# Performance work log

Hardware: AMD Instinct MI355X
Metric: run time of the kernel (lower is better)

## Reference

```python
import jax, jax.numpy as jnp
import numpy as np
from jax import lax

B, H, W, C = 8, 256, 256, 64
REDUCTION = 8
LENGTH = 9
HIDDEN = max(8, C // REDUCTION)


def _conv(x, w, b, pad='SAME'):
    y = lax.conv_general_dilated(x, w, (1, 1), pad,
                                 dimension_numbers=('NHWC', 'HWIO', 'NHWC'))
    return y + b


def _bilinear_sample(img, y, x):
    # img: [B,H,W,C]; y,x: [B,H,W] float coords
    Bi, Hi, Wi, _ = img.shape
    y0 = jnp.floor(y)
    x0 = jnp.floor(x)
    y0i = jnp.clip(y0.astype(jnp.int32), 0, Hi - 1)
    x0i = jnp.clip(x0.astype(jnp.int32), 0, Wi - 1)
    y1i = jnp.clip((y0 + 1.0).astype(jnp.int32), 0, Hi - 1)
    x1i = jnp.clip((x0 + 1.0).astype(jnp.int32), 0, Wi - 1)
    b = jnp.arange(Bi)[:, None, None]
    Ia = img[b, y0i, x0i]
    Ib = img[b, y1i, x0i]
    Ic = img[b, y0i, x1i]
    Id = img[b, y1i, x1i]
    # weights use CLIPPED integer corner coords (faithful to the TF source)
    y0f = y0i.astype(img.dtype)
    x0f = x0i.astype(img.dtype)
    y1f = y1i.astype(img.dtype)
    x1f = x1i.astype(img.dtype)
    wa = ((x1f - x) * (y1f - y))[..., None]
    wb = ((x1f - x) * (y - y0f))[..., None]
    wc = ((x - x0f) * (y1f - y))[..., None]
    wd = ((x - x0f) * (y - y0f))[..., None]
    return wa * Ia + wb * Ib + wc * Ic + wd * Id


def _oriented_pool(x, vx, vy):
    # x: [B,H,W,C]; vx,vy: [B,H,W] unit direction components
    _, Hi, Wi, _ = x.shape
    yy = jnp.arange(Hi, dtype=x.dtype)[None, :, None]  # broadcasts to [B,H,W]
    xx = jnp.arange(Wi, dtype=x.dtype)[None, None, :]
    half = LENGTH // 2
    acc = jnp.zeros_like(x)
    for t in range(-half, half + 1):  # fixed small set of offsets
        tf_ = jnp.asarray(t, dtype=x.dtype)
        cy = yy + tf_ * vy
        cx = xx + tf_ * vx
        acc = acc + _bilinear_sample(x, cy, cx)
    return acc / jnp.asarray(LENGTH, dtype=x.dtype)


def setup_inputs() -> dict:
    key = jax.random.key(0)
    ks = jax.random.split(key, 9)
    s = 0.05
    return {
        'x': jax.random.normal(ks[0], (B, H, W, C), jnp.float32),
        'w3': jax.random.normal(ks[1], (3, 3, C, HIDDEN), jnp.float32) * s,
        'b3': jnp.zeros((HIDDEN,), jnp.float32),
        'w1': jax.random.normal(ks[2], (1, 1, HIDDEN, 1), jnp.float32) * s,
        'b1': jnp.zeros((1,), jnp.float32),
        'wr': jax.random.normal(ks[3], (1, 1, 2 * C, HIDDEN), jnp.float32) * s,
        'br': jnp.zeros((HIDDEN,), jnp.float32),
        'we': jax.random.normal(ks[4], (1, 1, HIDDEN, 2 * C), jnp.float32) * s,
        'be': jnp.zeros((2 * C,), jnp.float32),
    }


def reference(x, w3, b3, w1, b1, wr, br, we, be):
    h = jax.nn.relu(_conv(x, w3, b3))                    # [B,H,W,hidden]
    theta = np.pi * jax.nn.sigmoid(_conv(h, w1, b1))     # [B,H,W,1]
    cos_t = jnp.cos(theta)[..., 0]                       # [B,H,W]
    sin_t = jnp.sin(theta)[..., 0]
    tan_feat = _oriented_pool(x, cos_t, sin_t)           # tangential direction
    nor_feat = _oriented_pool(x, -sin_t, cos_t)          # normal direction
    context = jnp.concatenate([tan_feat, nor_feat], axis=-1)  # [B,H,W,2C]
    r = jax.nn.relu(_conv(context, wr, br))
    w = jax.nn.sigmoid(_conv(r, we, be))                 # [B,H,W,2C]
    alpha_tan, alpha_norm = jnp.split(w, 2, axis=-1)
    return (alpha_tan + alpha_norm) * x
```

## Files before the change

### kernel.cpp

```cpp
#include <hip/hip_runtime.h>
#include <math.h>

#define PI_F 3.14159265358979323846f

typedef float f2 __attribute__((ext_vector_type(2)));

__device__ __forceinline__ f2 pkfma(f2 a, f2 b, f2 c) {
    return __builtin_elementwise_fma(a, b, c);
}
__device__ __forceinline__ f2 sp(float v) { f2 r; r.x = v; r.y = v; return r; }
__device__ __forceinline__ f2 mk2(float a, float b) { f2 r; r.x = a; r.y = b; return r; }

__device__ __forceinline__ float fold8h(float v0, float v1, float v2, float v3,
                                        float v4, float v5, float v6, float v7,
                                        int hl) {
    const bool b4 = (hl & 4) != 0;
    float k0 = b4 ? v4 : v0, g0 = b4 ? v0 : v4;
    float k1 = b4 ? v5 : v1, g1 = b4 ? v1 : v5;
    float k2 = b4 ? v6 : v2, g2 = b4 ? v2 : v6;
    float k3 = b4 ? v7 : v3, g3 = b4 ? v3 : v7;
    k0 += __shfl_xor(g0, 4, 64);
    k1 += __shfl_xor(g1, 4, 64);
    k2 += __shfl_xor(g2, 4, 64);
    k3 += __shfl_xor(g3, 4, 64);
    const bool b2 = (hl & 2) != 0;
    float m0 = b2 ? k2 : k0, n0 = b2 ? k0 : k2;
    float m1 = b2 ? k3 : k1, n1 = b2 ? k1 : k3;
    m0 += __shfl_xor(n0, 2, 64);
    m1 += __shfl_xor(n1, 2, 64);
    const bool b1_ = (hl & 1) != 0;
    float q = b1_ ? m1 : m0, r = b1_ ? m0 : m1;
    q += __shfl_xor(r, 1, 64);
    q += __shfl_xor(q, 8, 64);
    q += __shfl_xor(q, 16, 64);
    return q;
}

__global__ void repack_kernel(const float* __restrict__ w3,
                              const float* __restrict__ wr,
                              f2* __restrict__ ws) {
    int t = blockIdx.x * 256 + threadIdx.x;
    if (t < 2304) {
        int tap = t >> 8, rem = t & 255, hl = rem >> 3, j = rem & 7;
        f2 v; v.x = w3[((tap << 6) + (hl << 1)) * 8 + j];
        v.y = w3[((tap << 6) + (hl << 1) + 1) * 8 + j];
        ws[t] = v;
    } else if (t < 2560) {
        int rem = t - 2304, hl = rem >> 3, j = rem & 7;
        f2 v; v.x = wr[(hl << 1) * 8 + j];
        v.y = wr[((hl << 1) + 1) * 8 + j];
        ws[t] = v;
    } else if (t < 2816) {
        int rem = t - 2560, hl = rem >> 3, j = rem & 7;
        f2 v; v.x = wr[(64 + (hl << 1)) * 8 + j];
        v.y = wr[(64 + (hl << 1) + 1) * 8 + j];
        ws[t] = v;
    }
}

#define TR 11
#define TC 17

__device__ __forceinline__ f2 bilin_lds(const char* tb, float cy, float cx,
                                        int ybase, int xbase, unsigned laneoff,
                                        f2 acc) {
    int y0 = (int)floorf(cy), x0 = (int)floorf(cx);
    int y0i = min(max(y0, 0), 255);
    int y1i = min(max(y0 + 1, 0), 255);
    int x0i = min(max(x0, 0), 255);
    int x1i = min(max(x0 + 1, 0), 255);
    float wy0 = (float)y1i - cy, wy1 = cy - (float)y0i;
    float wx0 = (float)x1i - cx, wx1 = cx - (float)x0i;
    unsigned r0 = (unsigned)((y0i - ybase) * TC) << 8;
    unsigned r1 = (unsigned)((y1i - ybase) * TC) << 8;
    unsigned c0 = ((unsigned)(x0i - xbase) << 8) + laneoff;
    unsigned c1 = ((unsigned)(x1i - xbase) << 8) + laneoff;
    f2 Ia = *(const f2*)(tb + (r0 + c0));
    f2 Ib = *(const f2*)(tb + (r1 + c0));
    f2 Ic = *(const f2*)(tb + (r0 + c1));
    f2 Id = *(const f2*)(tb + (r1 + c1));
    acc = pkfma(sp(wx0 * wy0), Ia, acc);
    acc = pkfma(sp(wx0 * wy1), Ib, acc);
    acc = pkfma(sp(wx1 * wy0), Ic, acc);
    acc = pkfma(sp(wx1 * wy1), Id, acc);
    return acc;
}

__global__ __launch_bounds__(512) void oca_kernel(
    const float* __restrict__ x,
    const float* __restrict__ b3, const float* __restrict__ w1,
    const float* __restrict__ b1, const float* __restrict__ br,
    const float* __restrict__ we, const float* __restrict__ be,
    const f2* __restrict__ ws,
    float* __restrict__ out) {
    __shared__ float tile[TR * TC * 64];
    const int tid = threadIdx.x;
    const int lane = tid & 63;
    const int hl = lane & 31;
    const int half = lane >> 5;
    const int wid = __builtin_amdgcn_readfirstlane(tid >> 6);

    const unsigned beta = blockIdx.x;
    const int b   = beta >> 12;
    const int ty  = (beta >> 5) & 127;
    const int tx  = beta & 31;
    const int yq0 = ty << 1;
    const int xq0 = tx << 3;
    const int ybase = yq0 - 4;
    const int xbase = xq0 - 4;
    const float* xb = x + ((size_t)b << 22);

    {
        const int g   = tid >> 4;
        const int sub = (tid & 15) << 2;
        for (int p = g; p < TR * TC; p += 32) {
            int pr = p / TC;
            int pc = p - pr * TC;
            int gy = min(max(ybase + pr, 0), 255);
            int gx = min(max(xbase + pc, 0), 255);
            float4 v = *(const float4*)(xb + (size_t)(((gy << 8) + gx) << 6) + sub);
            *(float4*)((char*)tile + (p << 8) + (sub << 2)) = v;
        }
    }
    __syncthreads();

    const int yqw = yq0 + (wid >> 2);
    const int xql = xq0 + ((wid & 3) << 1) + half;
    const unsigned laneoff = (unsigned)hl << 3;
    const char* tb = (const char*)tile;

    f2 a0 = sp(0.f), a1 = sp(0.f), a2 = sp(0.f), a3 = sp(0.f);
    f2 a4 = sp(0.f), a5 = sp(0.f), a6 = sp(0.f), a7 = sp(0.f);
    f2 xc2 = sp(0.f);
#pragma unroll
    for (int dy = -1; dy <= 1; ++dy) {
#pragma unroll
        for (int dx = -1; dx <= 1; ++dx) {
            int yy = yqw + dy;
            int xx = xql + dx;
            bool valid = ((unsigned)yy < 256u) && ((unsigned)xx < 256u);
            int ry = min(max(yy, 0), 255) - ybase;
            int cx = min(max(xx, 0), 255) - xbase;
            f2 xv = *(const f2*)(tb + (((unsigned)(ry * TC + cx) << 8) + laneoff));
            xv = valid ? xv : sp(0.f);
            if (dy == 0 && dx == 0) xc2 = xv;
            const int tap = (dy + 1) * 3 + (dx + 1);
            const float4* wq = (const float4*)(ws + (tap << 8) + (hl << 3));
            float4 q0 = wq[0], q1 = wq[1], q2 = wq[2], q3 = wq[3];
            a0 = pkfma(xv, mk2(q0.x, q0.y), a0);
            a1 = pkfma(xv, mk2(q0.z, q0.w), a1);
            a2 = pkfma(xv, mk2(q1.x, q1.y), a2);
            a3 = pkfma(xv, mk2(q1.z, q1.w), a3);
            a4 = pkfma(xv, mk2(q2.x, q2.y), a4);
            a5 = pkfma(xv, mk2(q2.z, q2.w), a5);
            a6 = pkfma(xv, mk2(q3.x, q3.y), a6);
            a7 = pkfma(xv, mk2(q3.z, q3.w), a7);
        }
    }
    const int j = hl & 7;
    float hsum = fold8h(a0.x + a0.y, a1.x + a1.y, a2.x + a2.y, a3.x + a3.y,
                        a4.x + a4.y, a5.x + a5.y, a6.x + a6.y, a7.x + a7.y, hl);
    float h_l = fmaxf(hsum + b3[j], 0.f);

    float zp = h_l * w1[j];
    zp += __shfl_xor(zp, 1, 64);
    zp += __shfl_xor(zp, 2, 64);
    zp += __shfl_xor(zp, 4, 64);
    float z = zp + b1[0];
    float theta = PI_F * __builtin_amdgcn_rcpf(1.f + __expf(-z));
    float vcos = __cosf(theta);
    float vsin = __sinf(theta);

    const float fy = (float)yqw, fx = (float)xql;
    f2 at0 = sp(0.f), at1 = sp(0.f), an0 = sp(0.f), an1 = sp(0.f);
#pragma unroll
    for (int t = -4; t <= 4; ++t) {
        float tf = (float)t;
        f2& accT = (t & 1) ? at1 : at0;
        f2& accN = (t & 1) ? an1 : an0;
        accT = bilin_lds(tb, fmaf(tf, vsin, fy), fmaf(tf, vcos, fx),
                         ybase, xbase, laneoff, accT);
        accN = bilin_lds(tb, fmaf(tf, vcos, fy), fmaf(-tf, vsin, fx),
                         ybase, xbase, laneoff, accN);
    }
    f2 tan2 = mk2((at0.x + at1.x) * (1.f / 9.f), (at0.y + at1.y) * (1.f / 9.f));
    f2 nor2 = mk2((an0.x + an1.x) * (1.f / 9.f), (an0.y + an1.y) * (1.f / 9.f));

    const f2* wrp = ws + 2304 + (hl << 3);
    const f2* wrn = ws + 2560 + (hl << 3);
    f2 p0 = pkfma(tan2, wrp[0], sp(0.f)); p0 = pkfma(nor2, wrn[0], p0);
    f2 p1 = pkfma(tan2, wrp[1], sp(0.f)); p1 = pkfma(nor2, wrn[1], p1);
    f2 p2 = pkfma(tan2, wrp[2], sp(0.f)); p2 = pkfma(nor2, wrn[2], p2);
    f2 p3 = pkfma(tan2, wrp[3], sp(0.f)); p3 = pkfma(nor2, wrn[3], p3);
    f2 p4 = pkfma(tan2, wrp[4], sp(0.f)); p4 = pkfma(nor2, wrn[4], p4);
    f2 p5 = pkfma(tan2, wrp[5], sp(0.f)); p5 = pkfma(nor2, wrn[5], p5);
    f2 p6 = pkfma(tan2, wrp[6], sp(0.f)); p6 = pkfma(nor2, wrn[6], p6);
    f2 p7 = pkfma(tan2, wrp[7], sp(0.f)); p7 = pkfma(nor2, wrn[7], p7);
    float rsum = fold8h(p0.x + p0.y, p1.x + p1.y, p2.x + p2.y, p3.x + p3.y,
                        p4.x + p4.y, p5.x + p5.y, p6.x + p6.y, p7.x + p7.y, hl);
    float r_l = fmaxf(rsum + br[j], 0.f);

    float rb0 = r_l;
    float rb1 = __shfl_xor(rb0, 1, 64);
    float rb2 = __shfl_xor(rb0, 2, 64);
    float rb3 = __shfl_xor(rb1, 2, 64);
    float rb4 = __shfl_xor(rb0, 4, 64);
    float rb5 = __shfl_xor(rb1, 4, 64);
    float rb6 = __shfl_xor(rb2, 4, 64);
    float rb7 = __shfl_xor(rb3, 4, 64);

    const char* web = (const char*)we;
    unsigned voff = ((unsigned)j << 9) | laneoff;
    f2 zt2 = *(const f2*)((const char*)be + laneoff);
    f2 zn2 = *(const f2*)((const char*)be + 256 + laneoff);
#pragma unroll
    for (int m = 0; m < 8; ++m) {
        unsigned vm = voff ^ ((unsigned)m << 9);
        float rbm = (m == 0) ? rb0 : (m == 1) ? rb1 : (m == 2) ? rb2 : (m == 3) ? rb3
                  : (m == 4) ? rb4 : (m == 5) ? rb5 : (m == 6) ? rb6 : rb7;
        zt2 = pkfma(sp(rbm), *(const f2*)(web + vm), zt2);
        zn2 = pkfma(sp(rbm), *(const f2*)(web + vm + 256), zn2);
    }
    f2 wt2, wn2;
    wt2.x = __builtin_amdgcn_rcpf(1.f + __expf(-zt2.x));
    wt2.y = __builtin_amdgcn_rcpf(1.f + __expf(-zt2.y));
    wn2.x = __builtin_amdgcn_rcpf(1.f + __expf(-zn2.x));
    wn2.y = __builtin_amdgcn_rcpf(1.f + __expf(-zn2.y));

    f2 o = mk2((wt2.x + wn2.x) * xc2.x, (wt2.y + wn2.y) * xc2.y);
    size_t pixA = ((size_t)b << 16) + ((size_t)yqw << 8) + (size_t)(xq0 + ((wid & 3) << 1));
    *(f2*)((char*)out + (pixA << 8) + ((unsigned)lane << 3)) = o;
}

extern "C" void kernel_launch(void* const* d_in, const int* in_sizes, int n_in,
                              void* d_out, int out_size, void* d_ws, size_t ws_size,
                              hipStream_t stream) {
    const float* x  = (const float*)d_in[0];
    const float* w3 = (const float*)d_in[1];
    const float* b3 = (const float*)d_in[2];
    const float* w1 = (const float*)d_in[3];
    const float* b1 = (const float*)d_in[4];
    const float* wr = (const float*)d_in[5];
    const float* br = (const float*)d_in[6];
    const float* we = (const float*)d_in[7];
    const float* be = (const float*)d_in[8];
    float* out = (float*)d_out;
    f2* ws = (f2*)d_ws;

    repack_kernel<<<11, 256, 0, stream>>>(w3, wr, ws);

    dim3 grid(32768), block(512);
    oca_kernel<<<grid, block, 0, stream>>>(x, b3, w1, b1, br, we, be, ws, out);
}
```

Measured before the change: 1.069 ms.

## Store LDS tile as bf16, read conv taps from global, skip center sample

```diff
diff --git a/kernel.cpp b/kernel.cpp
--- a/kernel.cpp
+++ b/kernel.cpp
@@ -10,6 +10,13 @@
 }
 __device__ __forceinline__ f2 sp(float v) { f2 r; r.x = v; r.y = v; return r; }
 __device__ __forceinline__ f2 mk2(float a, float b) { f2 r; r.x = a; r.y = b; return r; }
+
+__device__ __forceinline__ f2 up2(unsigned u) {
+    f2 r;
+    r.x = __uint_as_float(u << 16);
+    r.y = __uint_as_float(u & 0xFFFF0000u);
+    return r;
+}
 
 __device__ __forceinline__ float fold8h(float v0, float v1, float v2, float v3,
                                         float v4, float v5, float v6, float v7,
@@ -61,9 +68,9 @@
 #define TR 11
 #define TC 17
 
-__device__ __forceinline__ f2 bilin_lds(const char* tb, float cy, float cx,
-                                        int ybase, int xbase, unsigned laneoff,
-                                        f2 acc) {
+__device__ __forceinline__ f2 samp(const char* tb, float cy, float cx,
+                                   int ybase, int xbase, unsigned laneoff4,
+                                   f2 acc) {
     int y0 = (int)floorf(cy), x0 = (int)floorf(cx);
     int y0i = min(max(y0, 0), 255);
     int y1i = min(max(y0 + 1, 0), 255);
@@ -71,18 +78,23 @@
     int x1i = min(max(x0 + 1, 0), 255);
     float wy0 = (float)y1i - cy, wy1 = cy - (float)y0i;
     float wx0 = (float)x1i - cx, wx1 = cx - (float)x0i;
-    unsigned r0 = (unsigned)((y0i - ybase) * TC) << 8;
-    unsigned r1 = (unsigned)((y1i - ybase) * TC) << 8;
-    unsigned c0 = ((unsigned)(x0i - xbase) << 8) + laneoff;
-    unsigned c1 = ((unsigned)(x1i - xbase) << 8) + laneoff;
-    f2 Ia = *(const f2*)(tb + (r0 + c0));
-    f2 Ib = *(const f2*)(tb + (r1 + c0));
-    f2 Ic = *(const f2*)(tb + (r0 + c1));
-    f2 Id = *(const f2*)(tb + (r1 + c1));
-    acc = pkfma(sp(wx0 * wy0), Ia, acc);
-    acc = pkfma(sp(wx0 * wy1), Ib, acc);
-    acc = pkfma(sp(wx1 * wy0), Ic, acc);
-    acc = pkfma(sp(wx1 * wy1), Id, acc);
+    if (x0 < 0) { wx0 = 0.f; wx1 = 0.f; }
+    unsigned rb0 = (unsigned)((y0i - ybase) * TC);
+    unsigned rb1 = (unsigned)((y1i - ybase) * TC);
+    unsigned c0 = (unsigned)(x0i - xbase);
+    unsigned c1 = (unsigned)(x1i - xbase);
+    unsigned a00 = ((rb0 + c0) << 7) + laneoff4;
+    unsigned a10 = ((rb1 + c0) << 7) + laneoff4;
+    unsigned a01 = ((rb0 + c1) << 7) + laneoff4;
+    unsigned a11 = ((rb1 + c1) << 7) + laneoff4;
+    unsigned u00 = *(const unsigned*)(tb + a00);
+    unsigned u10 = *(const unsigned*)(tb + a10);
+    unsigned u01 = *(const unsigned*)(tb + a01);
+    unsigned u11 = *(const unsigned*)(tb + a11);
+    acc = pkfma(sp(wx0 * wy0), up2(u00), acc);
+    acc = pkfma(sp(wx0 * wy1), up2(u10), acc);
+    acc = pkfma(sp(wx1 * wy0), up2(u01), acc);
+    acc = pkfma(sp(wx1 * wy1), up2(u11), acc);
     return acc;
 }
 
@@ -93,7 +105,7 @@
     const float* __restrict__ we, const float* __restrict__ be,
     const f2* __restrict__ ws,
     float* __restrict__ out) {
-    __shared__ float tile[TR * TC * 64];
+    __shared__ unsigned tile[TR * TC * 32];
     const int tid = threadIdx.x;
     const int lane = tid & 63;
     const int hl = lane & 31;
@@ -111,23 +123,29 @@
     const float* xb = x + ((size_t)b << 22);
 
     {
-        const int g   = tid >> 4;
-        const int sub = (tid & 15) << 2;
+        const int g    = tid >> 4;
+        const int subf = (tid & 15) << 2;
         for (int p = g; p < TR * TC; p += 32) {
             int pr = p / TC;
             int pc = p - pr * TC;
             int gy = min(max(ybase + pr, 0), 255);
             int gx = min(max(xbase + pc, 0), 255);
-            float4 v = *(const float4*)(xb + (size_t)(((gy << 8) + gx) << 6) + sub);
-            *(float4*)((char*)tile + (p << 8) + (sub << 2)) = v;
+            float4 v = *(const float4*)(xb + (size_t)(((gy << 8) + gx) << 6) + subf);
+            unsigned u0, u1;
+            asm("v_cvt_pk_bf16_f32 %0, %1, %2" : "=v"(u0) : "v"(v.x), "v"(v.y));
+            asm("v_cvt_pk_bf16_f32 %0, %1, %2" : "=v"(u1) : "v"(v.z), "v"(v.w));
+            uint2 wv; wv.x = u0; wv.y = u1;
+            *(uint2*)&tile[p * 32 + (subf >> 1)] = wv;
         }
     }
     __syncthreads();
 
     const int yqw = yq0 + (wid >> 2);
     const int xql = xq0 + ((wid & 3) << 1) + half;
-    const unsigned laneoff = (unsigned)hl << 3;
+    const unsigned laneoff8 = (unsigned)hl << 3;
+    const unsigned laneoff4 = (unsigned)hl << 2;
     const char* tb = (const char*)tile;
+    const char* xbb = (const char*)xb;
 
     f2 a0 = sp(0.f), a1 = sp(0.f), a2 = sp(0.f), a3 = sp(0.f);
     f2 a4 = sp(0.f), a5 = sp(0.f), a6 = sp(0.f), a7 = sp(0.f);
@@ -139,9 +157,9 @@
             int yy = yqw + dy;
             int xx = xql + dx;
             bool valid = ((unsigned)yy < 256u) && ((unsigned)xx < 256u);
-            int ry = min(max(yy, 0), 255) - ybase;
-            int cx = min(max(xx, 0), 255) - xbase;
-            f2 xv = *(const f2*)(tb + (((unsigned)(ry * TC + cx) << 8) + laneoff));
+            unsigned gy = (unsigned)min(max(yy, 0), 255);
+            unsigned gx = (unsigned)min(max(xx, 0), 255);
+            f2 xv = *(const f2*)(xbb + (((gy << 8) + gx) << 8) + laneoff8);
             xv = valid ? xv : sp(0.f);
             if (dy == 0 && dx == 0) xc2 = xv;
             const int tap = (dy + 1) * 3 + (dx + 1);
@@ -172,16 +190,19 @@
     float vsin = __sinf(theta);
 
     const float fy = (float)yqw, fx = (float)xql;
-    f2 at0 = sp(0.f), at1 = sp(0.f), an0 = sp(0.f), an1 = sp(0.f);
+    bool interior = (yqw < 255) && (xql < 255);
+    f2 t0c = interior ? xc2 : sp(0.f);
+    f2 at0 = t0c, at1 = sp(0.f), an0 = t0c, an1 = sp(0.f);
 #pragma unroll
     for (int t = -4; t <= 4; ++t) {
+        if (t == 0) continue;
         float tf = (float)t;
         f2& accT = (t & 1) ? at1 : at0;
         f2& accN = (t & 1) ? an1 : an0;
-        accT = bilin_lds(tb, fmaf(tf, vsin, fy), fmaf(tf, vcos, fx),
-                         ybase, xbase, laneoff, accT);
-        accN = bilin_lds(tb, fmaf(tf, vcos, fy), fmaf(-tf, vsin, fx),
-                         ybase, xbase, laneoff, accN);
+        accT = samp(tb, fmaf(tf, vsin, fy), fmaf(tf, vcos, fx),
+                    ybase, xbase, laneoff4, accT);
+        accN = samp(tb, fmaf(tf, vcos, fy), fmaf(-tf, vsin, fx),
+                    ybase, xbase, laneoff4, accN);
     }
     f2 tan2 = mk2((at0.x + at1.x) * (1.f / 9.f), (at0.y + at1.y) * (1.f / 9.f));
     f2 nor2 = mk2((an0.x + an1.x) * (1.f / 9.f), (an0.y + an1.y) * (1.f / 9.f));
@@ -210,9 +231,9 @@
     float rb7 = __shfl_xor(rb3, 4, 64);
 
     const char* web = (const char*)we;
-    unsigned voff = ((unsigned)j << 9) | laneoff;
-    f2 zt2 = *(const f2*)((const char*)be + laneoff);
-    f2 zn2 = *(const f2*)((const char*)be + 256 + laneoff);
+    unsigned voff = ((unsigned)j << 9) | laneoff8;
+    f2 zt2 = *(const f2*)((const char*)be + laneoff8);
+    f2 zn2 = *(const f2*)((const char*)be + 256 + laneoff8);
 #pragma unroll
     for (int m = 0; m < 8; ++m) {
         unsigned vm = voff ^ ((unsigned)m << 9);
```

Result: slower. 1.134 ms (+6.1%).
